# Kernel optimization log

Measured on AMD Instinct MI355X. Metric: run time of the kernel, lower is better.

The kernel has to match this reference:

```python
import jax, jax.numpy as jnp
import numpy as np

EPS = 1.1920929e-07  # torch nn.RMSNorm default eps = finfo(fp32).eps
H, NOPE, ROPE, VD = 16, 128, 64, 128
QKD = NOPE + ROPE


def rmsnorm(x, w):
    return x * jax.lax.rsqrt(jnp.mean(x * x, axis=-1, keepdims=True) + EPS) * w


def rope(x, cos, sin):
    # x: [B,S,h,D]; cos/sin broadcast to [B,S,h,D//2]; pairs are (even, odd) interleaved
    x2 = x.reshape(*x.shape[:-1], -1, 2)
    x0, x1 = x2[..., 0], x2[..., 1]
    r = x0 * cos - x1 * sin
    i = x0 * sin + x1 * cos
    return jnp.stack([r, i], axis=-1).reshape(x.shape)


def setup_inputs() -> dict:
    key = jax.random.key(0)
    ks = jax.random.split(key, 8)
    B, S, D = 2, 2048, 2048
    QR, KR = 1536, 512
    x = jax.random.normal(ks[0], (B, S, D), jnp.float32)
    # RoPE table: theta=10000, rope dim 64 -> 32 frequencies
    pos = np.arange(S)[:, None]
    inv = 1.0 / (10000.0 ** (np.arange(0, ROPE, 2) / ROPE))[None, :]
    ang = pos * inv
    freqs_cos = jnp.asarray(np.cos(ang), jnp.float32)
    freqs_sin = jnp.asarray(np.sin(ang), jnp.float32)

    def w(k, out_dim, in_dim):
        return jax.random.normal(k, (out_dim, in_dim), jnp.float32) / np.sqrt(in_dim)

    return {
        "x": x,
        "freqs_cos": freqs_cos,
        "freqs_sin": freqs_sin,
        "Wq_down": w(ks[1], QR, D),
        "q_norm_w": jnp.ones((QR,), jnp.float32),
        "Wq_up": w(ks[2], H * QKD, QR),
        "Wkv_down": w(ks[3], ROPE + KR, D),
        "kv_norm_w": jnp.ones((KR,), jnp.float32),
        "Wkv_up": w(ks[4], H * (VD + NOPE), KR),
        "Wo": w(ks[5], D, H * VD),
        "bo": jnp.zeros((D,), jnp.float32),
        "start_pos": 0,
    }


def reference(x, freqs_cos, freqs_sin, Wq_down, q_norm_w, Wq_up, Wkv_down, kv_norm_w, Wkv_up, Wo, bo, start_pos):
    B, S, D = x.shape
    cos = freqs_cos[None, :, None, :]
    sin = freqs_sin[None, :, None, :]
    # low-rank Q path: down -> RMSNorm -> up
    q = rmsnorm(x @ Wq_down.T, q_norm_w) @ Wq_up.T
    q = q.reshape(B, S, H, QKD)
    q_nope, q_rope = q[..., :NOPE], q[..., NOPE:]
    q_rope = rope(q_rope, cos, sin)
    q = jnp.concatenate([q_nope, q_rope], axis=-1)  # [B,S,H,QKD]
    # low-rank KV path: shared rope part + latent kv
    kv = x @ Wkv_down.T
    k_rope, c_kv = kv[..., :ROPE], kv[..., ROPE:]
    k_rope = rope(k_rope[:, :, None, :], cos, sin)  # [B,S,1,ROPE]
    kv = rmsnorm(c_kv, kv_norm_w) @ Wkv_up.T
    kv = kv.reshape(B, S, H, NOPE + VD)
    k_nope, v = kv[..., :NOPE], kv[..., NOPE:]
    k = jnp.concatenate([k_nope, jnp.broadcast_to(k_rope, (B, S, H, ROPE))], axis=-1)
    # causal SDPA (start_pos=0 prefill: cache slice equals fresh K/V)
    scale = 1.0 / np.sqrt(QKD)
    scores = jnp.einsum("bqhd,bkhd->bhqk", q, k) * scale
    mask = jnp.tril(jnp.ones((S, S), bool))
    scores = jnp.where(mask, scores, -jnp.inf)
    attn = jax.nn.softmax(scores, axis=-1)
    o = jnp.einsum("bhqk,bkhd->bqhd", attn, v).reshape(B, S, H * VD)
    return o @ Wo.T + bo
```

## Files before the change

### kernel.cpp

```cpp
#include <hip/hip_runtime.h>
#include <hip/hip_bf16.h>
#include <stdint.h>


typedef short bf16x8 __attribute__((ext_vector_type(8)));
typedef float f32x4  __attribute__((ext_vector_type(4)));
typedef unsigned int u32;

#define RMS_EPS 1.1920929e-07f
#define SCALE_L2E 0.10411931095f

__device__ __forceinline__ unsigned short f2b(float f) {
  union { float f; uint32_t u; } c; c.f = f;
  uint32_t u = c.u;
  return (unsigned short)((u + 0x7FFFu + ((u >> 16) & 1u)) >> 16);
}
__device__ __forceinline__ float b2f(short s) {
  union { uint32_t u; float f; } c; c.u = ((uint32_t)(unsigned short)s) << 16;
  return c.f;
}
__device__ __forceinline__ u32 pk2(float a, float b) {
  union { __hip_bfloat162 h; u32 u; } cv;
  cv.h = __float22bfloat162_rn(float2{a, b});
  return cv.u;
}
__device__ __forceinline__ void gld16(const short* g, short* l) {
  __builtin_amdgcn_global_load_lds(
      (const __attribute__((address_space(1))) u32*)g,
      (__attribute__((address_space(3))) u32*)l, 16, 0, 0);
}

__device__ __forceinline__ void cvt4(const float* __restrict__ in,
                                     short* __restrict__ out, int i) {
  float4 v = ((const float4*)in)[i];
  union { ushort4 s; uint2 u; } o;
  o.s.x = f2b(v.x); o.s.y = f2b(v.y); o.s.z = f2b(v.z); o.s.w = f2b(v.w);
  ((uint2*)out)[i] = o.u;
}

__global__ void f2bf_all_kernel(
    const float* __restrict__ x,    short* __restrict__ x_bf,
    const float* __restrict__ Wqd,  short* __restrict__ w_qd,
    const float* __restrict__ Wqu,  short* __restrict__ w_qu,
    const float* __restrict__ Wkvu, short* __restrict__ w_kvu,
    const float* __restrict__ Wo,   short* __restrict__ w_o,
    const float* __restrict__ Wkvd, short* __restrict__ w_kvd) {
  int i = blockIdx.x * 256 + threadIdx.x;
  if (i < 2097152) { cvt4(x, x_bf, i); return; }
  i -= 2097152;
  if (i < 786432) { cvt4(Wqd, w_qd, i); return; }
  i -= 786432;
  if (i < 1179648) { cvt4(Wqu, w_qu, i); return; }
  i -= 1179648;
  if (i < 524288) { cvt4(Wkvu, w_kvu, i); return; }
  i -= 524288;
  if (i < 1048576) { cvt4(Wo, w_o, i); return; }
  i -= 1048576;
  if (i >= 327680) return;
  int row = i >> 9;
  ushort4 s = {0, 0, 0, 0};
  if (row < 576) {
    float4 v = ((const float4*)Wkvd)[i];
    s.x = f2b(v.x); s.y = f2b(v.y); s.z = f2b(v.z); s.w = f2b(v.w);
  }
  union { ushort4 ss; uint2 u; } o; o.ss = s;
  ((uint2*)w_kvd)[i] = o.u;
}

template <int EPI>
__global__ __launch_bounds__(256) void gemm_bt(
    const short* __restrict__ A, const short* __restrict__ Bt,
    void* __restrict__ Cv, const float* __restrict__ bias,
    int K, int ldc,
    const float* __restrict__ fc, const float* __restrict__ fs,
    short* __restrict__ aux) {
  __shared__ __align__(16) short As[128 * 32];
  __shared__ __align__(16) short Bs[128 * 32];
  int nx = gridDim.x;
  int lin = blockIdx.y * nx + blockIdx.x;
  int cpx = (nx * gridDim.y) >> 3;
  int swz = (lin & 7) * cpx + (lin >> 3);
  int row0 = (swz / nx) * 128, col0 = (swz % nx) * 128;
  int t = threadIdx.x, lane = t & 63, w = t >> 6;
  int wm = w >> 1, wn = w & 1;
  int l15 = lane & 15, l4 = lane >> 4;
  f32x4 acc[4][4] = {};

  int srow = lane >> 2, scol = (lane & 3) * 8;
  const short* Ag = A + (size_t)(row0 + srow) * K + scol;
  const short* Bg = Bt + (size_t)(col0 + srow) * K + scol;

  for (int kt = 0; kt < K; kt += 32) {
#pragma unroll
    for (int c = 0; c < 2; ++c) {
      int blk = w * 2 + c;
      gld16(Ag + (size_t)(blk * 16) * K + kt, As + blk * 512);
      gld16(Bg + (size_t)(blk * 16) * K + kt, Bs + blk * 512);
    }
    __syncthreads();
    bf16x8 af[4], bfr[4];
#pragma unroll
    for (int i = 0; i < 4; ++i) {
      af[i]  = *(const bf16x8*)(As + (wm * 64 + i * 16 + l15) * 32 + l4 * 8);
      bfr[i] = *(const bf16x8*)(Bs + (wn * 64 + i * 16 + l15) * 32 + l4 * 8);
    }
#pragma unroll
    for (int i = 0; i < 4; ++i)
#pragma unroll
      for (int j = 0; j < 4; ++j) {
        if constexpr (EPI == 3)
          acc[i][j] = __builtin_amdgcn_mfma_f32_16x16x32_bf16(af[i], bfr[j], acc[i][j], 0, 0, 0);
        else
          acc[i][j] = __builtin_amdgcn_mfma_f32_16x16x32_bf16(bfr[j], af[i], acc[i][j], 0, 0, 0);
      }
    __syncthreads();
  }

  if constexpr (EPI == 0) {
    float* C = (float*)Cv;
#pragma unroll
    for (int i = 0; i < 4; ++i) {
      int row = row0 + wm * 64 + i * 16 + l15;
#pragma unroll
      for (int j = 0; j < 4; ++j) {
        int coln = col0 + wn * 64 + j * 16 + l4 * 4;
        float4 bv = {0.f, 0.f, 0.f, 0.f};
        if (bias) bv = *(const float4*)(bias + coln);
        float4 o;
        o.x = acc[i][j][0] + bv.x; o.y = acc[i][j][1] + bv.y;
        o.z = acc[i][j][2] + bv.z; o.w = acc[i][j][3] + bv.w;
        *(float4*)(C + (size_t)row * ldc + coln) = o;
      }
    }
  } else if constexpr (EPI == 1) {
    short* C = (short*)Cv;
#pragma unroll
    for (int i = 0; i < 4; ++i) {
      int row = row0 + wm * 64 + i * 16 + l15;
#pragma unroll
      for (int j = 0; j < 4; ++j) {
        int coln = col0 + wn * 64 + j * 16 + l4 * 4;
        uint2 o;
        o.x = pk2(acc[i][j][0], acc[i][j][1]);
        o.y = pk2(acc[i][j][2], acc[i][j][3]);
        *(uint2*)(C + (size_t)row * ldc + coln) = o;
      }
    }
  } else if constexpr (EPI == 2) {
    short* qb = (short*)Cv;
#pragma unroll
    for (int i = 0; i < 4; ++i) {
      int row = row0 + wm * 64 + i * 16 + l15;
      int b = row >> 11, s = row & 2047;
#pragma unroll
      for (int j = 0; j < 4; ++j) {
        int coln = col0 + wn * 64 + j * 16 + l4 * 4;
        int h = coln / 192;
        int d0 = coln - h * 192;
        float v0 = acc[i][j][0], v1 = acc[i][j][1];
        float v2 = acc[i][j][2], v3 = acc[i][j][3];
        float o0, o1, o2, o3;
        if (d0 >= 128) {
          int ir0 = (d0 - 128) >> 1;
          float c0 = fc[s * 32 + ir0], s0 = fs[s * 32 + ir0];
          float c1 = fc[s * 32 + ir0 + 1], s1 = fs[s * 32 + ir0 + 1];
          o0 = v0 * c0 - v1 * s0; o1 = v0 * s0 + v1 * c0;
          o2 = v2 * c1 - v3 * s1; o3 = v2 * s1 + v3 * c1;
        } else {
          o0 = v0; o1 = v1; o2 = v2; o3 = v3;
        }
        uint2 o;
        o.x = pk2(o0 * SCALE_L2E, o1 * SCALE_L2E);
        o.y = pk2(o2 * SCALE_L2E, o3 * SCALE_L2E);
        *(uint2*)(qb + ((size_t)((b * 16 + h) * 2048 + s)) * 192 + d0) = o;
      }
    }
  } else {
    short* kb = (short*)Cv;
    short* vT = aux;
    int h = col0 >> 8;
    if ((col0 & 128) == 0) {
#pragma unroll
      for (int j = 0; j < 4; ++j) {
        int d = wn * 64 + j * 16 + l15;
#pragma unroll
        for (int i = 0; i < 4; ++i) {
          int rowb = row0 + wm * 64 + i * 16 + l4 * 4;
#pragma unroll
          for (int r = 0; r < 4; ++r) {
            int row = rowb + r;
            int b = row >> 11, s = row & 2047;
            kb[((size_t)((b * 16 + h) * 2048 + s)) * 128 + d] = (short)f2b(acc[i][j][r]);
          }
        }
      }
    } else {
#pragma unroll
      for (int j = 0; j < 4; ++j) {
        int dv = wn * 64 + j * 16 + l15;
#pragma unroll
        for (int i = 0; i < 4; ++i) {
          int s0 = row0 + wm * 64 + i * 16 + l4 * 4;
          int b = s0 >> 11, s = s0 & 2047;
          short4 o;
          o.x = (short)f2b(acc[i][j][0]);
          o.y = (short)f2b(acc[i][j][1]);
          o.z = (short)f2b(acc[i][j][2]);
          o.w = (short)f2b(acc[i][j][3]);
          *(short4*)(vT + ((size_t)((b * 16 + h) * 128 + dv)) * 2048 + s) = o;
        }
      }
    }
  }
}

template <int W>
__device__ __forceinline__ void rms_body(
    const short* __restrict__ in, const float* __restrict__ wgt,
    short* __restrict__ out, int ld_in, int blk) {
  constexpr int NC = W / 512;
  int row = blk * 4 + (threadIdx.x >> 6);
  int lane = threadIdx.x & 63;
  const short* x = in + (size_t)row * ld_in + lane * 8;
  float vals[NC * 8];
  float ss = 0.f;
#pragma unroll
  for (int c = 0; c < NC; ++c) {
    bf16x8 v = *(const bf16x8*)(x + c * 512);
#pragma unroll
    for (int k = 0; k < 8; ++k) {
      float f = b2f(v[k]);
      vals[c * 8 + k] = f; ss += f * f;
    }
  }
#pragma unroll
  for (int off = 32; off > 0; off >>= 1) ss += __shfl_xor(ss, off);
  float rs = rsqrtf(ss / (float)W + RMS_EPS);
  short* o = out + (size_t)row * W + lane * 8;
#pragma unroll
  for (int c = 0; c < NC; ++c) {
    const float4* wp = (const float4*)(wgt + c * 512 + lane * 8);
    float4 w0 = wp[0], w1 = wp[1];
    ushort4 lo, hi;
    lo.x = f2b(vals[c * 8 + 0] * rs * w0.x);
    lo.y = f2b(vals[c * 8 + 1] * rs * w0.y);
    lo.z = f2b(vals[c * 8 + 2] * rs * w0.z);
    lo.w = f2b(vals[c * 8 + 3] * rs * w0.w);
    hi.x = f2b(vals[c * 8 + 4] * rs * w1.x);
    hi.y = f2b(vals[c * 8 + 5] * rs * w1.y);
    hi.z = f2b(vals[c * 8 + 6] * rs * w1.z);
    hi.w = f2b(vals[c * 8 + 7] * rs * w1.w);
    *(ushort4*)(o + c * 512) = lo;
    *(ushort4*)(o + c * 512 + 4) = hi;
  }
}

__global__ __launch_bounds__(256) void norm_krope_kernel(
    const short* __restrict__ c1,
    const float* __restrict__ qnw, short* __restrict__ qn,
    const float* __restrict__ kvnw, short* __restrict__ ckvn,
    const float* __restrict__ fc, const float* __restrict__ fs,
    short* __restrict__ kr) {
  int bb = blockIdx.x;
  if (bb < 1024) {
    rms_body<1536>(c1, qnw, qn, 2176, bb);
  } else if (bb < 2048) {
    rms_body<512>(c1 + 1600, kvnw, ckvn, 2176, bb - 1024);
  } else {
    int idx = (bb - 2048) * 256 + threadIdx.x;
    int i = idx & 31;
    int s = (idx >> 5) & 2047;
    int b = idx >> 16;
    const short* row = c1 + (size_t)(b * 2048 + s) * 2176 + 1536 + 2 * i;
    float x0 = b2f(row[0]), x1 = b2f(row[1]);
    float c = fc[s * 32 + i], sn = fs[s * 32 + i];
    uint32_t pk = (uint32_t)f2b(x0 * c - x1 * sn) | ((uint32_t)f2b(x0 * sn + x1 * c) << 16);
    *(uint32_t*)(kr + ((size_t)(b * 2048 + s)) * 64 + 2 * i) = pk;
  }
}

__global__ __launch_bounds__(256) void attn_kernel(
    const short* __restrict__ qb, const short* __restrict__ kb,
    const short* __restrict__ kr, const short* __restrict__ vtb,
    short* __restrict__ ob) {
  __shared__ __align__(16) short Ks[64 * 196];
  __shared__ __align__(16) short Vs[128 * 70];
  int bid = blockIdx.x;
  int xcd = bid & 7, kk2 = bid >> 3;
  int bh = xcd * 4 + (kk2 >> 4);
  int qx = kk2 & 15;
  int b = bh >> 4, h = bh & 15;
  int t = threadIdx.x, lane = t & 63, w = t >> 6;
  int l15 = lane & 15, l4 = lane >> 4;
  const short* Kbh = kb + (size_t)bh * 2048 * 128;
  const short* krb = kr + (size_t)b * 2048 * 64;
  const short* Vbh = vtb + (size_t)bh * 128 * 2048;

  int kn_r = t >> 4, kn_c = (t & 15) * 8;
  int kr_r = t >> 3, kr_c = (t & 7) * 8;
  int v_d = t >> 3, v_c = (t & 7) * 8;

  int sA = (l15 + ((l4 & 1) << 5)) << 2;
  int sB = sA + (16 << 2);
  bool chi = (l4 >> 1) != 0;

  for (int half = 0; half < 2; ++half) {
    int qt = half ? (31 - qx) : qx;
    int q0 = qt * 64;
    const short* Qbase = qb + ((size_t)bh * 2048 + q0 + w * 16) * 192;
    bf16x8 qf[6];
#pragma unroll
    for (int kk = 0; kk < 6; ++kk)
      qf[kk] = *(const bf16x8*)(Qbase + (size_t)l15 * 192 + kk * 32 + l4 * 8);
    f32x4 oaccT[8] = {};
    float m_i = -1e30f, l_i = 0.f;
    int qcol = q0 + w * 16 + l15;
    int kend = q0 + 64;

    for (int kt = 0; kt < kend; kt += 64) {
#pragma unroll
      for (int c = 0; c < 4; ++c) {
        int r = kn_r + 16 * c;
        *(bf16x8*)(Ks + r * 196 + kn_c) =
            *(const bf16x8*)(Kbh + (size_t)(kt + r) * 128 + kn_c);
      }
#pragma unroll
      for (int c = 0; c < 2; ++c) {
        int r = kr_r + 32 * c;
        *(bf16x8*)(Ks + r * 196 + 128 + kr_c) =
            *(const bf16x8*)(krb + (size_t)(kt + r) * 64 + kr_c);
      }
#pragma unroll
      for (int c = 0; c < 4; ++c) {
        int d = v_d + 32 * c;
        *(bf16x8*)(Vs + d * 70 + v_c) =
            *(const bf16x8*)(Vbh + (size_t)d * 2048 + kt + v_c);
      }
      __syncthreads();

      f32x4 s[4] = {};
      __builtin_amdgcn_s_setprio(1);
#pragma unroll
      for (int kk = 0; kk < 6; ++kk) {
#pragma unroll
        for (int c = 0; c < 4; ++c) {
          bf16x8 kf = *(const bf16x8*)(Ks + (c * 16 + l15) * 196 + kk * 32 + l4 * 8);
          s[c] = __builtin_amdgcn_mfma_f32_16x16x32_bf16(kf, qf[kk], s[c], 0, 0, 0);
        }
      }
      __builtin_amdgcn_s_setprio(0);

      if (kt == q0) {
#pragma unroll
        for (int c = 0; c < 4; ++c)
#pragma unroll
          for (int r = 0; r < 4; ++r) {
            int k = kt + c * 16 + l4 * 4 + r;
            if (k > qcol) s[c][r] = -1e30f;
          }
      }
      float mx = fmaxf(fmaxf(fmaxf(s[0][0], s[0][1]), fmaxf(s[0][2], s[0][3])),
                       fmaxf(fmaxf(s[1][0], s[1][1]), fmaxf(s[1][2], s[1][3])));
      mx = fmaxf(mx, fmaxf(fmaxf(fmaxf(s[2][0], s[2][1]), fmaxf(s[2][2], s[2][3])),
                           fmaxf(fmaxf(s[3][0], s[3][1]), fmaxf(s[3][2], s[3][3]))));
      mx = fmaxf(mx, __shfl_xor(mx, 16));
      mx = fmaxf(mx, __shfl_xor(mx, 32));
      float newm = fmaxf(m_i, mx);
      float alpha = __builtin_amdgcn_exp2f(m_i - newm);
      float rs = 0.f;
#pragma unroll
      for (int c = 0; c < 4; ++c)
#pragma unroll
        for (int r = 0; r < 4; ++r) {
          float p = __builtin_amdgcn_exp2f(s[c][r] - newm);
          s[c][r] = p; rs += p;
        }
      rs += __shfl_xor(rs, 16);
      rs += __shfl_xor(rs, 32);
      l_i = l_i * alpha + rs;
      m_i = newm;
#pragma unroll
      for (int dt = 0; dt < 8; ++dt)
#pragma unroll
        for (int r = 0; r < 4; ++r) oaccT[dt][r] *= alpha;

      u32 pk00 = pk2(s[0][0], s[0][1]), pk01 = pk2(s[0][2], s[0][3]);
      u32 pk10 = pk2(s[1][0], s[1][1]), pk11 = pk2(s[1][2], s[1][3]);
      u32 pk20 = pk2(s[2][0], s[2][1]), pk21 = pk2(s[2][2], s[2][3]);
      u32 pk30 = pk2(s[3][0], s[3][1]), pk31 = pk2(s[3][2], s[3][3]);
      union { bf16x8 v; u32 u[4]; } P0, P1;
      {
        u32 a0 = __builtin_amdgcn_ds_bpermute(sA, (int)pk00);
        u32 a1 = __builtin_amdgcn_ds_bpermute(sA, (int)pk01);
        u32 a2 = __builtin_amdgcn_ds_bpermute(sB, (int)pk00);
        u32 a3 = __builtin_amdgcn_ds_bpermute(sB, (int)pk01);
        u32 b0 = __builtin_amdgcn_ds_bpermute(sA, (int)pk10);
        u32 b1 = __builtin_amdgcn_ds_bpermute(sA, (int)pk11);
        u32 b2 = __builtin_amdgcn_ds_bpermute(sB, (int)pk10);
        u32 b3 = __builtin_amdgcn_ds_bpermute(sB, (int)pk11);
        P0.u[0] = chi ? b0 : a0; P0.u[1] = chi ? b1 : a1;
        P0.u[2] = chi ? b2 : a2; P0.u[3] = chi ? b3 : a3;
      }
      {
        u32 a0 = __builtin_amdgcn_ds_bpermute(sA, (int)pk20);
        u32 a1 = __builtin_amdgcn_ds_bpermute(sA, (int)pk21);
        u32 a2 = __builtin_amdgcn_ds_bpermute(sB, (int)pk20);
        u32 a3 = __builtin_amdgcn_ds_bpermute(sB, (int)pk21);
        u32 b0 = __builtin_amdgcn_ds_bpermute(sA, (int)pk30);
        u32 b1 = __builtin_amdgcn_ds_bpermute(sA, (int)pk31);
        u32 b2 = __builtin_amdgcn_ds_bpermute(sB, (int)pk30);
        u32 b3 = __builtin_amdgcn_ds_bpermute(sB, (int)pk31);
        P1.u[0] = chi ? b0 : a0; P1.u[1] = chi ? b1 : a1;
        P1.u[2] = chi ? b2 : a2; P1.u[3] = chi ? b3 : a3;
      }

      __builtin_amdgcn_s_setprio(1);
#pragma unroll
      for (int dt = 0; dt < 8; ++dt) {
        bf16x8 vf0 = *(const bf16x8*)(Vs + (dt * 16 + l15) * 70 + l4 * 8);
        bf16x8 vf1 = *(const bf16x8*)(Vs + (dt * 16 + l15) * 70 + 32 + l4 * 8);
        oaccT[dt] = __builtin_amdgcn_mfma_f32_16x16x32_bf16(vf0, P0.v, oaccT[dt], 0, 0, 0);
        oaccT[dt] = __builtin_amdgcn_mfma_f32_16x16x32_bf16(vf1, P1.v, oaccT[dt], 0, 0, 0);
      }
      __builtin_amdgcn_s_setprio(0);
      __syncthreads();
    }
    float inv = 1.0f / l_i;
    short* dst = ob + ((size_t)(b * 2048 + qcol)) * 2048 + h * 128;
#pragma unroll
    for (int dt = 0; dt < 8; ++dt) {
      uint2 o;
      o.x = pk2(oaccT[dt][0] * inv, oaccT[dt][1] * inv);
      o.y = pk2(oaccT[dt][2] * inv, oaccT[dt][3] * inv);
      *(uint2*)(dst + dt * 16 + l4 * 4) = o;
    }
  }
}

extern "C" void kernel_launch(void* const* d_in, const int* in_sizes, int n_in,
                              void* d_out, int out_size, void* d_ws, size_t ws_size,
                              hipStream_t stream) {
  const float* x    = (const float*)d_in[0];
  const float* fcos = (const float*)d_in[1];
  const float* fsin = (const float*)d_in[2];
  const float* Wqd  = (const float*)d_in[3];
  const float* qnw  = (const float*)d_in[4];
  const float* Wqu  = (const float*)d_in[5];
  const float* Wkvd = (const float*)d_in[6];
  const float* kvnw = (const float*)d_in[7];
  const float* Wkvu = (const float*)d_in[8];
  const float* Wo   = (const float*)d_in[9];
  const float* bo   = (const float*)d_in[10];
  float* out = (float*)d_out;
  char* ws = (char*)d_ws;

  short* x_bf  = (short*)(ws + 0);
  short* w_cat = (short*)(ws + 16777216);
  short* w_qu  = (short*)(ws + 25690112);
  short* w_kvu = (short*)(ws + 35127296);
  short* w_o   = (short*)(ws + 39321600);
  short* c1    = (short*)(ws + 47710208);
  short* qn    = (short*)(ws + 65536000);
  short* ckvn  = (short*)(ws + 78118912);
  short* q_b   = (short*)(ws + 82313216);
  short* k_b   = (short*)(ws + 107479040);
  short* vT    = (short*)(ws + 132644864);
  short* o_bf  = (short*)(ws + 149422080);
  short* kr    = (short*)(ws + 166199296);

  f2bf_all_kernel<<<23296, 256, 0, stream>>>(x, x_bf, Wqd, w_cat, Wqu, w_qu,
                                             Wkvu, w_kvu, Wo, w_o,
                                             Wkvd, w_cat + 1536 * 2048);

  gemm_bt<1><<<dim3(17, 32), 256, 0, stream>>>(x_bf, w_cat, c1, nullptr, 2048, 2176,
                                               nullptr, nullptr, nullptr);
  norm_krope_kernel<<<2560, 256, 0, stream>>>(c1, qnw, qn, kvnw, ckvn,
                                              fcos, fsin, kr);

  gemm_bt<2><<<dim3(24, 32), 256, 0, stream>>>(qn, w_qu, q_b, nullptr, 1536, 0,
                                               fcos, fsin, nullptr);
  gemm_bt<3><<<dim3(32, 32), 256, 0, stream>>>(ckvn, w_kvu, k_b, nullptr, 512, 0,
                                               nullptr, nullptr, vT);

  attn_kernel<<<512, 256, 0, stream>>>(q_b, k_b, kr, vT, o_bf);

  gemm_bt<0><<<dim3(16, 32), 256, 0, stream>>>(o_bf, w_o, out, bo, 2048, 2048,
                                               nullptr, nullptr, nullptr);
}
```

Before: 356.8 us.

## Merge Q/KV up-projection GEMMs and register-prefetch next K/V tile in attention

The two independent up-projection GEMMs (Q with RoPE epilogue, KV with V-transpose epilogue) are merged into one launch that splits its 1792 blocks by index, so one kernel's tail no longer serializes before the other starts. The GEMM body is refactored into a device function for this. In attention, the next K, k_rope and V tile is loaded into registers right after the barrier so global latency overlaps the MFMA work, and launch bounds request two blocks per SIMD. The prefetch raises register pressure, and the occupancy hint may force spills.

```diff
diff --git a/kernel.cpp b/kernel.cpp
--- a/kernel.cpp
+++ b/kernel.cpp
@@ -68,19 +68,13 @@
 }
 
 template <int EPI>
-__global__ __launch_bounds__(256) void gemm_bt(
+__device__ __forceinline__ void gemm_body(
+    short* As, short* Bs, int row0, int col0,
     const short* __restrict__ A, const short* __restrict__ Bt,
     void* __restrict__ Cv, const float* __restrict__ bias,
     int K, int ldc,
     const float* __restrict__ fc, const float* __restrict__ fs,
     short* __restrict__ aux) {
-  __shared__ __align__(16) short As[128 * 32];
-  __shared__ __align__(16) short Bs[128 * 32];
-  int nx = gridDim.x;
-  int lin = blockIdx.y * nx + blockIdx.x;
-  int cpx = (nx * gridDim.y) >> 3;
-  int swz = (lin & 7) * cpx + (lin >> 3);
-  int row0 = (swz / nx) * 128, col0 = (swz % nx) * 128;
   int t = threadIdx.x, lane = t & 63, w = t >> 6;
   int wm = w >> 1, wn = w & 1;
   int l15 = lane & 15, l4 = lane >> 4;
@@ -211,6 +205,46 @@
         }
       }
     }
+  }
+}
+
+template <int EPI>
+__global__ __launch_bounds__(256) void gemm_bt(
+    const short* __restrict__ A, const short* __restrict__ Bt,
+    void* __restrict__ Cv, const float* __restrict__ bias,
+    int K, int ldc,
+    const float* __restrict__ fc, const float* __restrict__ fs,
+    short* __restrict__ aux) {
+  __shared__ __align__(16) short As[128 * 32];
+  __shared__ __align__(16) short Bs[128 * 32];
+  int nx = gridDim.x;
+  int lin = blockIdx.y * nx + blockIdx.x;
+  int cpx = (nx * gridDim.y) >> 3;
+  int swz = (lin & 7) * cpx + (lin >> 3);
+  int row0 = (swz / nx) * 128, col0 = (swz % nx) * 128;
+  gemm_body<EPI>(As, Bs, row0, col0, A, Bt, Cv, bias, K, ldc, fc, fs, aux);
+}
+
+__global__ __launch_bounds__(256) void gemm_up(
+    const short* __restrict__ qn, const short* __restrict__ wqu,
+    short* __restrict__ q_b,
+    const short* __restrict__ ckvn, const short* __restrict__ wkvu,
+    short* __restrict__ k_b, short* __restrict__ vT,
+    const float* __restrict__ fc, const float* __restrict__ fs) {
+  __shared__ __align__(16) short As[128 * 32];
+  __shared__ __align__(16) short Bs[128 * 32];
+  int bb = blockIdx.x;
+  if (bb < 768) {
+    int cpx = 768 >> 3;
+    int swz = (bb & 7) * cpx + (bb >> 3);
+    int row0 = (swz / 24) * 128, col0 = (swz % 24) * 128;
+    gemm_body<2>(As, Bs, row0, col0, qn, wqu, q_b, nullptr, 1536, 0, fc, fs, nullptr);
+  } else {
+    int bb2 = bb - 768;
+    int cpx = 1024 >> 3;
+    int swz = (bb2 & 7) * cpx + (bb2 >> 3);
+    int row0 = (swz / 32) * 128, col0 = (swz % 32) * 128;
+    gemm_body<3>(As, Bs, row0, col0, ckvn, wkvu, k_b, nullptr, 512, 0, nullptr, nullptr, vT);
   }
 }
 
@@ -279,7 +313,7 @@
   }
 }
 
-__global__ __launch_bounds__(256) void attn_kernel(
+__global__ __launch_bounds__(256, 2) void attn_kernel(
     const short* __restrict__ qb, const short* __restrict__ kb,
     const short* __restrict__ kr, const short* __restrict__ vtb,
     short* __restrict__ ob) {
@@ -317,26 +351,43 @@
     int qcol = q0 + w * 16 + l15;
     int kend = q0 + 64;
 
+    bf16x8 pn0, pn1, pn2, pn3, pr0, pr1, pv0, pv1, pv2, pv3;
+    pn0 = *(const bf16x8*)(Kbh + (size_t)(kn_r) * 128 + kn_c);
+    pn1 = *(const bf16x8*)(Kbh + (size_t)(kn_r + 16) * 128 + kn_c);
+    pn2 = *(const bf16x8*)(Kbh + (size_t)(kn_r + 32) * 128 + kn_c);
+    pn3 = *(const bf16x8*)(Kbh + (size_t)(kn_r + 48) * 128 + kn_c);
+    pr0 = *(const bf16x8*)(krb + (size_t)(kr_r) * 64 + kr_c);
+    pr1 = *(const bf16x8*)(krb + (size_t)(kr_r + 32) * 64 + kr_c);
+    pv0 = *(const bf16x8*)(Vbh + (size_t)(v_d) * 2048 + v_c);
+    pv1 = *(const bf16x8*)(Vbh + (size_t)(v_d + 32) * 2048 + v_c);
+    pv2 = *(const bf16x8*)(Vbh + (size_t)(v_d + 64) * 2048 + v_c);
+    pv3 = *(const bf16x8*)(Vbh + (size_t)(v_d + 96) * 2048 + v_c);
+
     for (int kt = 0; kt < kend; kt += 64) {
-#pragma unroll
-      for (int c = 0; c < 4; ++c) {
-        int r = kn_r + 16 * c;
-        *(bf16x8*)(Ks + r * 196 + kn_c) =
-            *(const bf16x8*)(Kbh + (size_t)(kt + r) * 128 + kn_c);
-      }
-#pragma unroll
-      for (int c = 0; c < 2; ++c) {
-        int r = kr_r + 32 * c;
-        *(bf16x8*)(Ks + r * 196 + 128 + kr_c) =
-            *(const bf16x8*)(krb + (size_t)(kt + r) * 64 + kr_c);
-      }
-#pragma unroll
-      for (int c = 0; c < 4; ++c) {
-        int d = v_d + 32 * c;
-        *(bf16x8*)(Vs + d * 70 + v_c) =
-            *(const bf16x8*)(Vbh + (size_t)d * 2048 + kt + v_c);
-      }
+      *(bf16x8*)(Ks + (kn_r) * 196 + kn_c) = pn0;
+      *(bf16x8*)(Ks + (kn_r + 16) * 196 + kn_c) = pn1;
+      *(bf16x8*)(Ks + (kn_r + 32) * 196 + kn_c) = pn2;
+      *(bf16x8*)(Ks + (kn_r + 48) * 196 + kn_c) = pn3;
+      *(bf16x8*)(Ks + (kr_r) * 196 + 128 + kr_c) = pr0;
+      *(bf16x8*)(Ks + (kr_r + 32) * 196 + 128 + kr_c) = pr1;
+      *(bf16x8*)(Vs + (v_d) * 70 + v_c) = pv0;
+      *(bf16x8*)(Vs + (v_d + 32) * 70 + v_c) = pv1;
+      *(bf16x8*)(Vs + (v_d + 64) * 70 + v_c) = pv2;
+      *(bf16x8*)(Vs + (v_d + 96) * 70 + v_c) = pv3;
       __syncthreads();
+      if (kt + 64 < kend) {
+        int k2 = kt + 64;
+        pn0 = *(const bf16x8*)(Kbh + (size_t)(k2 + kn_r) * 128 + kn_c);
+        pn1 = *(const bf16x8*)(Kbh + (size_t)(k2 + kn_r + 16) * 128 + kn_c);
+        pn2 = *(const bf16x8*)(Kbh + (size_t)(k2 + kn_r + 32) * 128 + kn_c);
+        pn3 = *(const bf16x8*)(Kbh + (size_t)(k2 + kn_r + 48) * 128 + kn_c);
+        pr0 = *(const bf16x8*)(krb + (size_t)(k2 + kr_r) * 64 + kr_c);
+        pr1 = *(const bf16x8*)(krb + (size_t)(k2 + kr_r + 32) * 64 + kr_c);
+        pv0 = *(const bf16x8*)(Vbh + (size_t)(v_d) * 2048 + k2 + v_c);
+        pv1 = *(const bf16x8*)(Vbh + (size_t)(v_d + 32) * 2048 + k2 + v_c);
+        pv2 = *(const bf16x8*)(Vbh + (size_t)(v_d + 64) * 2048 + k2 + v_c);
+        pv3 = *(const bf16x8*)(Vbh + (size_t)(v_d + 96) * 2048 + k2 + v_c);
+      }
 
       f32x4 s[4] = {};
       __builtin_amdgcn_s_setprio(1);
@@ -477,10 +528,8 @@
   norm_krope_kernel<<<2560, 256, 0, stream>>>(c1, qnw, qn, kvnw, ckvn,
                                               fcos, fsin, kr);
 
-  gemm_bt<2><<<dim3(24, 32), 256, 0, stream>>>(qn, w_qu, q_b, nullptr, 1536, 0,
-                                               fcos, fsin, nullptr);
-  gemm_bt<3><<<dim3(32, 32), 256, 0, stream>>>(ckvn, w_kvu, k_b, nullptr, 512, 0,
-                                               nullptr, nullptr, vT);
+  gemm_up<<<1792, 256, 0, stream>>>(qn, w_qu, q_b, ckvn, w_kvu, k_b, vT,
+                                    fcos, fsin);
 
   attn_kernel<<<512, 256, 0, stream>>>(q_b, k_b, kr, vT, o_bf);
 
```

After: 351.3 us. Within noise of the previous version (-1.5%).
